# Performance work log

Hardware: AMD Instinct MI355X
Metric: run time of the kernel (lower is better)

The kernel has to match this reference:

```python
import jax, jax.numpy as jnp
import numpy as np

NUM_NODE = 5000
EMBED_DIM = 256
NUM_CLS = 20
EDGE_ROWS = (NUM_NODE - 1) * (NUM_NODE - 1) + 1  # 24990002
BZ, SEQ, NBR = 64, 512, 16


def setup_inputs() -> dict:
    key = jax.random.key(0)
    k = jax.random.split(key, 8)
    X = jax.random.randint(k[0], (BZ, SEQ), 0, NUM_NODE)
    NX = jax.random.randint(k[1], (BZ, SEQ, NBR), 0, NUM_NODE)
    EW = jax.random.randint(k[2], (BZ, SEQ, NBR), 0, EDGE_ROWS)
    # parameters (xavier-ish scale); padding_idx=0 rows zeroed
    node_emb = jax.random.normal(k[3], (NUM_NODE, EMBED_DIM), jnp.float32) * 0.02
    node_emb = node_emb.at[0].set(0.0)
    edge_w = jax.random.normal(k[4], (EDGE_ROWS, 1), jnp.float32) * 0.02
    edge_w = edge_w.at[0].set(0.0)
    node_w = jax.random.normal(k[5], (NUM_NODE, 1), jnp.float32) * 0.02
    node_w = node_w.at[0].set(0.0)
    fc_W = jax.random.normal(k[6], (NUM_CLS, EMBED_DIM), jnp.float32) * 0.05
    fc_b = jnp.zeros((NUM_CLS,), jnp.float32)
    return {"X": X, "NX": NX, "EW": EW, "node_emb": node_emb,
            "edge_w": edge_w, "node_w": node_w, "fc_W": fc_W, "fc_b": fc_b}


def reference(X, NX, EW, node_emb, edge_w, node_w, fc_W, fc_b):
    Ra = node_emb[NX]                      # (bz, seq, nbr, d) neighbor embeddings
    Ean = edge_w[EW]                       # (bz, seq, nbr, 1) edge weights
    Mn = jnp.max(Ra * Ean, axis=2)         # (bz, seq, d) max over neighbors
    Rn = node_emb[X]                       # (bz, seq, d)
    Nn = node_w[X]                         # (bz, seq, 1)
    y = (1.0 - Nn) * Mn + Nn * Rn          # weighted combine
    y = jnp.sum(y, axis=1)                 # (bz, d) sum-pool over sequence
    y = y @ fc_W.T + fc_b                  # (bz, num_cls)
    y = jax.nn.relu(y)
    # Dropout is identity at inference; LogSoftmax over dim=1
    return jax.nn.log_softmax(y, axis=1)
```

## Files before the change

### kernel.cpp

```cpp
#include <hip/hip_runtime.h>
#include <math.h>

#define BZ   64
#define SEQ  512
#define NBR  16
#define DIM  256
#define NCLS 20

#define SEQ_PER_BLOCK 16
#define WAVES 4

__global__ __launch_bounds__(256) void zero_ws_kernel(float* __restrict__ ws, int n) {
    int i = blockIdx.x * blockDim.x + threadIdx.x;
    if (i < n) ws[i] = 0.0f;
}

__global__ __launch_bounds__(256) void gnn_gather_kernel(
    const int*   __restrict__ X,
    const int*   __restrict__ NX,
    const int*   __restrict__ EW,
    const float* __restrict__ node_emb,
    const float* __restrict__ edge_w,
    const float* __restrict__ node_w,
    float*       __restrict__ ypre)
{
    __shared__ float lds[WAVES][DIM];

    const int nchunks = SEQ / SEQ_PER_BLOCK;
    const int b     = blockIdx.x / nchunks;
    const int chunk = blockIdx.x % nchunks;
    const int wave  = threadIdx.x >> 6;
    const int lane  = threadIdx.x & 63;

    float4 acc = make_float4(0.f, 0.f, 0.f, 0.f);

    #pragma unroll
    for (int i = 0; i < SEQ_PER_BLOCK / WAVES; ++i) {
        const int s  = chunk * SEQ_PER_BLOCK + wave * (SEQ_PER_BLOCK / WAVES) + i;
        const int bs = b * SEQ + s;

        int   nx = 0;
        float ew = 0.f;
        if (lane < NBR) {
            nx = NX[bs * NBR + lane];
            ew = edge_w[EW[bs * NBR + lane]];
        }

        float4 m = make_float4(-INFINITY, -INFINITY, -INFINITY, -INFINITY);
        #pragma unroll
        for (int k = 0; k < NBR; ++k) {
            const int   n = __shfl(nx, k);
            const float w = __shfl(ew, k);
            const float4 e = *(const float4*)(node_emb + (size_t)n * DIM + 4 * lane);
            m.x = fmaxf(m.x, e.x * w);
            m.y = fmaxf(m.y, e.y * w);
            m.z = fmaxf(m.z, e.z * w);
            m.w = fmaxf(m.w, e.w * w);
        }

        const int   x  = X[bs];
        const float nn = node_w[x];
        const float om = 1.0f - nn;
        const float4 r = *(const float4*)(node_emb + (size_t)x * DIM + 4 * lane);

        acc.x += om * m.x + nn * r.x;
        acc.y += om * m.y + nn * r.y;
        acc.z += om * m.z + nn * r.z;
        acc.w += om * m.w + nn * r.w;
    }

    *(float4*)&lds[wave][4 * lane] = acc;
    __syncthreads();

    const int t = threadIdx.x;
    const float sum = lds[0][t] + lds[1][t] + lds[2][t] + lds[3][t];
    atomicAdd(&ypre[b * DIM + t], sum);
}

__global__ __launch_bounds__(64) void gnn_head_kernel(
    const float* __restrict__ ypre,
    const float* __restrict__ fc_W,
    const float* __restrict__ fc_b,
    float*       __restrict__ out)
{
    __shared__ float yrow[DIM];
    __shared__ float vals[NCLS];
    __shared__ float lse;

    const int b = blockIdx.x;
    const int t = threadIdx.x;

    ((float4*)yrow)[t] = ((const float4*)(ypre + b * DIM))[t];
    __syncthreads();

    if (t < NCLS) {
        float a = fc_b[t];
        const float* w = fc_W + t * DIM;
        #pragma unroll 4
        for (int d = 0; d < DIM; ++d) a += yrow[d] * w[d];
        vals[t] = fmaxf(a, 0.0f);
    }
    __syncthreads();

    if (t == 0) {
        float mx = -INFINITY;
        for (int c = 0; c < NCLS; ++c) mx = fmaxf(mx, vals[c]);
        float s = 0.0f;
        for (int c = 0; c < NCLS; ++c) s += expf(vals[c] - mx);
        lse = mx + logf(s);
    }
    __syncthreads();

    if (t < NCLS) out[b * NCLS + t] = vals[t] - lse;
}

extern "C" void kernel_launch(void* const* d_in, const int* in_sizes, int n_in,
                              void* d_out, int out_size, void* d_ws, size_t ws_size,
                              hipStream_t stream) {
    const int*   X        = (const int*)  d_in[0];
    const int*   NX       = (const int*)  d_in[1];
    const int*   EW       = (const int*)  d_in[2];
    const float* node_emb = (const float*)d_in[3];
    const float* edge_w   = (const float*)d_in[4];
    const float* node_w   = (const float*)d_in[5];
    const float* fc_W     = (const float*)d_in[6];
    const float* fc_b     = (const float*)d_in[7];
    float* out  = (float*)d_out;
    float* ypre = (float*)d_ws;

    zero_ws_kernel<<<(BZ * DIM + 255) / 256, 256, 0, stream>>>(ypre, BZ * DIM);

    gnn_gather_kernel<<<BZ * (SEQ / SEQ_PER_BLOCK), 256, 0, stream>>>(
        X, NX, EW, node_emb, edge_w, node_w, ypre);

    gnn_head_kernel<<<BZ, 64, 0, stream>>>(ypre, fc_W, fc_b, out);
}
```

Before: 211.4 us.

## Batch index loads per wave, use readlane broadcasts, replace atomics with partial slots

Each wave now loads the neighbor and edge indices for all four of its sequence positions at once, using full 64 lanes with nontemporal loads. It broadcasts them with readlane instead of shuffles, so the per-position dependent load chains are removed. When the workspace is large enough, per-chunk partial sums go to separate slots, which drops the zeroing kernel and the atomics, and the head kernel reduces those slots with 256 threads and a wave-reduction dot product. Launch bounds now request 4 blocks per CU to raise occupancy, at some cost in register budget.

```diff
diff --git a/kernel.cpp b/kernel.cpp
--- a/kernel.cpp
+++ b/kernel.cpp
@@ -8,61 +8,70 @@
 #define NCLS 20
 
 #define SEQ_PER_BLOCK 16
-#define WAVES 4
+#define NCHUNK (SEQ / SEQ_PER_BLOCK)
+
+__device__ __forceinline__ int bcast_i(int v, int lane) {
+    return __builtin_amdgcn_readlane(v, lane);
+}
+__device__ __forceinline__ float bcast_f(float v, int lane) {
+    return __int_as_float(__builtin_amdgcn_readlane(__float_as_int(v), lane));
+}
 
 __global__ __launch_bounds__(256) void zero_ws_kernel(float* __restrict__ ws, int n) {
     int i = blockIdx.x * blockDim.x + threadIdx.x;
     if (i < n) ws[i] = 0.0f;
 }
 
-__global__ __launch_bounds__(256) void gnn_gather_kernel(
+__global__ __launch_bounds__(256, 4) void gnn_gather_kernel(
     const int*   __restrict__ X,
     const int*   __restrict__ NX,
     const int*   __restrict__ EW,
     const float* __restrict__ node_emb,
     const float* __restrict__ edge_w,
     const float* __restrict__ node_w,
-    float*       __restrict__ ypre)
+    float*       __restrict__ dst,
+    int use_atomic)
 {
-    __shared__ float lds[WAVES][DIM];
+    __shared__ float lds[4][DIM];
 
-    const int nchunks = SEQ / SEQ_PER_BLOCK;
-    const int b     = blockIdx.x / nchunks;
-    const int chunk = blockIdx.x % nchunks;
+    const int b     = blockIdx.x / NCHUNK;
+    const int chunk = blockIdx.x % NCHUNK;
     const int wave  = threadIdx.x >> 6;
     const int lane  = threadIdx.x & 63;
+
+    const int s0  = chunk * SEQ_PER_BLOCK + wave * 4;
+    const int bs0 = b * SEQ + s0;
+
+    const int   nx  = __builtin_nontemporal_load(&NX[bs0 * NBR + lane]);
+    const int   ewi = __builtin_nontemporal_load(&EW[bs0 * NBR + lane]);
+    const float ew  = __builtin_nontemporal_load(&edge_w[ewi]);
+
+    int   xv  = 0;
+    float nwv = 0.f;
+    if (lane < 4) {
+        xv  = X[bs0 + lane];
+        nwv = node_w[xv];
+    }
 
     float4 acc = make_float4(0.f, 0.f, 0.f, 0.f);
 
     #pragma unroll
-    for (int i = 0; i < SEQ_PER_BLOCK / WAVES; ++i) {
-        const int s  = chunk * SEQ_PER_BLOCK + wave * (SEQ_PER_BLOCK / WAVES) + i;
-        const int bs = b * SEQ + s;
-
-        int   nx = 0;
-        float ew = 0.f;
-        if (lane < NBR) {
-            nx = NX[bs * NBR + lane];
-            ew = edge_w[EW[bs * NBR + lane]];
-        }
-
+    for (int p = 0; p < 4; ++p) {
         float4 m = make_float4(-INFINITY, -INFINITY, -INFINITY, -INFINITY);
         #pragma unroll
         for (int k = 0; k < NBR; ++k) {
-            const int   n = __shfl(nx, k);
-            const float w = __shfl(ew, k);
+            const int   n = bcast_i(nx, p * 16 + k);
+            const float w = bcast_f(ew, p * 16 + k);
             const float4 e = *(const float4*)(node_emb + (size_t)n * DIM + 4 * lane);
             m.x = fmaxf(m.x, e.x * w);
             m.y = fmaxf(m.y, e.y * w);
             m.z = fmaxf(m.z, e.z * w);
             m.w = fmaxf(m.w, e.w * w);
         }
-
-        const int   x  = X[bs];
-        const float nn = node_w[x];
+        const int   x  = bcast_i(xv, p);
+        const float nn = bcast_f(nwv, p);
         const float om = 1.0f - nn;
         const float4 r = *(const float4*)(node_emb + (size_t)x * DIM + 4 * lane);
-
         acc.x += om * m.x + nn * r.x;
         acc.y += om * m.y + nn * r.y;
         acc.z += om * m.z + nn * r.z;
@@ -74,14 +83,19 @@
 
     const int t = threadIdx.x;
     const float sum = lds[0][t] + lds[1][t] + lds[2][t] + lds[3][t];
-    atomicAdd(&ypre[b * DIM + t], sum);
+    if (use_atomic) {
+        atomicAdd(&dst[b * DIM + t], sum);
+    } else {
+        dst[(b * NCHUNK + chunk) * DIM + t] = sum;
+    }
 }
 
-__global__ __launch_bounds__(64) void gnn_head_kernel(
-    const float* __restrict__ ypre,
+__global__ __launch_bounds__(256) void gnn_head_kernel(
+    const float* __restrict__ part,
     const float* __restrict__ fc_W,
     const float* __restrict__ fc_b,
-    float*       __restrict__ out)
+    float*       __restrict__ out,
+    int nslots)
 {
     __shared__ float yrow[DIM];
     __shared__ float vals[NCLS];
@@ -90,15 +104,24 @@
     const int b = blockIdx.x;
     const int t = threadIdx.x;
 
-    ((float4*)yrow)[t] = ((const float4*)(ypre + b * DIM))[t];
+    float sum = 0.f;
+    for (int c = 0; c < nslots; ++c)
+        sum += part[((size_t)b * nslots + c) * DIM + t];
+    yrow[t] = sum;
     __syncthreads();
 
-    if (t < NCLS) {
-        float a = fc_b[t];
-        const float* w = fc_W + t * DIM;
-        #pragma unroll 4
-        for (int d = 0; d < DIM; ++d) a += yrow[d] * w[d];
-        vals[t] = fmaxf(a, 0.0f);
+    const int wave = t >> 6;
+    const int lane = t & 63;
+    const float4 y4 = *(const float4*)&yrow[4 * lane];
+
+    #pragma unroll
+    for (int ci = 0; ci < 5; ++ci) {
+        const int c = wave * 5 + ci;
+        const float4 w4 = *(const float4*)(fc_W + c * DIM + 4 * lane);
+        float d = y4.x * w4.x + y4.y * w4.y + y4.z * w4.z + y4.w * w4.w;
+        #pragma unroll
+        for (int off = 32; off; off >>= 1) d += __shfl_xor(d, off);
+        if (lane == 0) vals[c] = fmaxf(d + fc_b[c], 0.0f);
     }
     __syncthreads();
 
@@ -125,13 +148,20 @@
     const float* node_w   = (const float*)d_in[5];
     const float* fc_W     = (const float*)d_in[6];
     const float* fc_b     = (const float*)d_in[7];
-    float* out  = (float*)d_out;
-    float* ypre = (float*)d_ws;
+    float* out = (float*)d_out;
+    float* ws  = (float*)d_ws;
 
-    zero_ws_kernel<<<(BZ * DIM + 255) / 256, 256, 0, stream>>>(ypre, BZ * DIM);
+    const size_t need = (size_t)BZ * NCHUNK * DIM * sizeof(float);
+    const int use_atomic = (ws_size < need) ? 1 : 0;
 
-    gnn_gather_kernel<<<BZ * (SEQ / SEQ_PER_BLOCK), 256, 0, stream>>>(
-        X, NX, EW, node_emb, edge_w, node_w, ypre);
-
-    gnn_head_kernel<<<BZ, 64, 0, stream>>>(ypre, fc_W, fc_b, out);
+    if (use_atomic) {
+        zero_ws_kernel<<<(BZ * DIM + 255) / 256, 256, 0, stream>>>(ws, BZ * DIM);
+        gnn_gather_kernel<<<BZ * NCHUNK, 256, 0, stream>>>(
+            X, NX, EW, node_emb, edge_w, node_w, ws, 1);
+        gnn_head_kernel<<<BZ, 256, 0, stream>>>(ws, fc_W, fc_b, out, 1);
+    } else {
+        gnn_gather_kernel<<<BZ * NCHUNK, 256, 0, stream>>>(
+            X, NX, EW, node_emb, edge_w, node_w, ws, 0);
+        gnn_head_kernel<<<BZ, 256, 0, stream>>>(ws, fc_W, fc_b, out, NCHUNK);
+    }
 }
```

After: 192.4 us. -9.0%, faster.
